# Kernel tuning notes

Measured on AMD Instinct MI355X. Metric: run time of the kernel, lower is better.

## Reference

```python
import jax, jax.numpy as jnp
import numpy as np

B, T, C = 2, 2048, 1024
N_HEAD = 16
HEAD_DIM = C // N_HEAD


def setup_inputs() -> dict:
    key = jax.random.key(0)
    k1, k2, k3 = jax.random.split(key, 3)
    s = 1.0 / np.sqrt(C)
    return {
        "x": jax.random.normal(k1, (B, T, C), dtype=jnp.float32),
        "w_qkv": jax.random.normal(k2, (C, 3 * C), dtype=jnp.float32) * s,
        "b_qkv": jnp.zeros((3 * C,), dtype=jnp.float32),
        "w_out": jax.random.normal(k3, (C, C), dtype=jnp.float32) * s,
        "b_out": jnp.zeros((C,), dtype=jnp.float32),
    }


def reference(x, w_qkv, b_qkv, w_out, b_out):
    b, t, c = x.shape
    qkv = x @ w_qkv + b_qkv                                   # [B,T,3C]
    # Faithful to torch: view(B,T,H,3*hd).transpose(1,2) then split last dim
    qkv = qkv.reshape(b, t, N_HEAD, 3 * HEAD_DIM).transpose(0, 2, 1, 3)  # [B,H,T,3hd]
    q, k, v = jnp.split(qkv, 3, axis=-1)                      # each [B,H,T,hd]
    att = jnp.einsum("bhqd,bhkd->bhqk", q, k) / np.sqrt(HEAD_DIM)
    causal = jnp.tril(jnp.ones((t, t), dtype=bool))
    att = jnp.where(causal[None, None], att, -jnp.inf)
    att = jax.nn.softmax(att, axis=-1)                        # dropout p=0 (eval)
    y = jnp.einsum("bhqk,bhkd->bhqd", att, v)                 # [B,H,T,hd]
    y = y.transpose(0, 2, 1, 3).reshape(b, t, c)
    return y @ w_out + b_out
```

## Files before the change

kernel.cpp:

```cpp
#include <hip/hip_runtime.h>


#define T_SEQ 2048
#define C_DIM 1024
#define NH    16
#define HD    64
#define BT    4096

typedef short bf16x8 __attribute__((ext_vector_type(8)));
typedef float floatx4 __attribute__((ext_vector_type(4)));

static __device__ __forceinline__ unsigned short f2bf(float f) {
    union { float f; unsigned u; } v; v.f = f;
    unsigned u = v.u;
    return (unsigned short)((u + 0x7FFFu + ((u >> 16) & 1u)) >> 16);
}
static __device__ __forceinline__ float bf2f(unsigned short u) {
    union { unsigned u; float f; } v; v.u = ((unsigned)u) << 16; return v.f;
}

static __device__ __forceinline__ void gl2lds16(const void* g, void* l) {
    __builtin_amdgcn_global_load_lds(
        (const __attribute__((address_space(1))) unsigned int*)g,
        (__attribute__((address_space(3))) unsigned int*)l, 16, 0, 0);
}

static __device__ __forceinline__ void transpose_body(float (*tile)[65],
                                                      const float* __restrict__ W,
                                                      unsigned short* __restrict__ Wt,
                                                      int K, int N, int bx, int by) {
    const int k0 = by << 6;
    const int n0 = bx << 6;
    const int rr = threadIdx.x >> 4;
    const int cc = (threadIdx.x & 15) << 2;
#pragma unroll
    for (int i = 0; i < 4; i++) {
        int r = rr + (i << 4);
        *(float4*)&tile[r][cc] = *(const float4*)(W + (size_t)(k0 + r) * N + n0 + cc);
    }
    __syncthreads();
#pragma unroll
    for (int i = 0; i < 4; i++) {
        int nr = rr + (i << 4);
        ushort4 o;
        o.x = f2bf(tile[cc + 0][nr]);
        o.y = f2bf(tile[cc + 1][nr]);
        o.z = f2bf(tile[cc + 2][nr]);
        o.w = f2bf(tile[cc + 3][nr]);
        *(ushort4*)(Wt + (size_t)(n0 + nr) * K + k0 + cc) = o;
    }
}

__global__ __launch_bounds__(256) void prep(const float* __restrict__ x,
                                            unsigned short* __restrict__ xb,
                                            const float* __restrict__ w_qkv,
                                            unsigned short* __restrict__ wqkvT,
                                            const float* __restrict__ w_out,
                                            unsigned short* __restrict__ woutT) {
    __shared__ float tile[64][65];
    const int bx = blockIdx.x;
    if (bx < 1024) {
        int i = (bx * 256 + threadIdx.x) * 4;
        const int n = BT * C_DIM;
        const int stride = 1024 * 1024;
        for (; i < n; i += stride) {
            float4 f = *(const float4*)(x + i);
            ushort4 o;
            o.x = f2bf(f.x); o.y = f2bf(f.y); o.z = f2bf(f.z); o.w = f2bf(f.w);
            *(ushort4*)(xb + i) = o;
        }
    } else if (bx < 1024 + 768) {
        int b = bx - 1024;
        transpose_body(tile, w_qkv, wqkvT, 1024, 3072, b % 48, b / 48);
    } else {
        int b = bx - 1024 - 768;
        transpose_body(tile, w_out, woutT, 1024, 1024, b % 16, b / 16);
    }
}

__global__ __launch_bounds__(256) void transp_v(const unsigned short* __restrict__ vb,
                                                unsigned short* __restrict__ vt) {
    __shared__ unsigned short tile[64][68];
    const int t0 = blockIdx.x << 6;
    const int bh = blockIdx.y;
    const size_t base = (size_t)bh * T_SEQ * HD;
    const int r = threadIdx.x >> 3;
    const int c = (threadIdx.x & 7) << 3;
#pragma unroll
    for (int i = 0; i < 2; i++) {
        const unsigned short* src = vb + base + (size_t)(t0 + r + (i << 5)) * HD + c;
        ushort4 u0 = *(const ushort4*)src;
        ushort4 u1 = *(const ushort4*)(src + 4);
        *(ushort4*)&tile[r + (i << 5)][c] = u0;
        *(ushort4*)&tile[r + (i << 5)][c + 4] = u1;
    }
    __syncthreads();
#pragma unroll
    for (int i = 0; i < 2; i++) {
        int s = threadIdx.x + (i << 8);
        int d = s >> 3;
        int tc = (s & 7) << 3;
        ushort4 o0, o1;
        o0.x = tile[tc + 0][d]; o0.y = tile[tc + 1][d];
        o0.z = tile[tc + 2][d]; o0.w = tile[tc + 3][d];
        o1.x = tile[tc + 4][d]; o1.y = tile[tc + 5][d];
        o1.z = tile[tc + 6][d]; o1.w = tile[tc + 7][d];
        unsigned short* dst = vt + ((size_t)bh * HD + d) * T_SEQ + t0 + tc;
        *(ushort4*)dst = o0;
        *(ushort4*)(dst + 4) = o1;
    }
}

#define GEMM_CORE(A_, Bt_, K_)                                                      \
    __shared__ short As[128 * 64];                                                  \
    __shared__ short Bs[128 * 64];                                                  \
    const int tid  = threadIdx.x;                                                   \
    const int lane = tid & 63, wave = tid >> 6;                                     \
    const int ln   = lane & 15, quad = lane >> 4;                                   \
    const int wm   = wave & 1,  wn   = wave >> 1;                                   \
    const int row0 = blockIdx.y << 7;                                               \
    const int col0 = blockIdx.x << 7;                                               \
    floatx4 acc[4][4];                                                              \
    _Pragma("unroll")                                                               \
    for (int i = 0; i < 4; i++)                                                     \
        _Pragma("unroll")                                                           \
        for (int j = 0; j < 4; j++) acc[i][j] = (floatx4){0.f, 0.f, 0.f, 0.f};      \
    for (int k0 = 0; k0 < K_; k0 += 64) {                                           \
        _Pragma("unroll")                                                           \
        for (int i = 0; i < 4; i++) {                                               \
            int c = (i << 8) + tid;                                                 \
            int r = c >> 3;                                                         \
            int gsrc = (c & 7) ^ (r & 7);                                           \
            gl2lds16(A_  + (size_t)(row0 + r) * K_ + k0 + (gsrc << 3), &As[c << 3]); \
            gl2lds16(Bt_ + (size_t)(col0 + r) * K_ + k0 + (gsrc << 3), &Bs[c << 3]); \
        }                                                                           \
        __syncthreads();                                                            \
        _Pragma("unroll")                                                           \
        for (int half = 0; half < 2; half++) {                                      \
            bf16x8 af[4], bfr[4];                                                   \
            _Pragma("unroll")                                                       \
            for (int t4 = 0; t4 < 4; t4++) {                                        \
                int ra = (wm << 6) + (t4 << 4) + ln;                                \
                int rb = (wn << 6) + (t4 << 4) + ln;                                \
                int g  = (half << 2) + quad;                                        \
                af[t4]  = *(bf16x8*)&As[((ra << 3) + (g ^ (ra & 7))) << 3];         \
                bfr[t4] = *(bf16x8*)&Bs[((rb << 3) + (g ^ (rb & 7))) << 3];         \
            }                                                                       \
            _Pragma("unroll")                                                       \
            for (int mt = 0; mt < 4; mt++)                                          \
                _Pragma("unroll")                                                   \
                for (int nt = 0; nt < 4; nt++)                                      \
                    acc[mt][nt] = __builtin_amdgcn_mfma_f32_16x16x32_bf16(af[mt], bfr[nt], acc[mt][nt], 0, 0, 0); \
        }                                                                           \
        __syncthreads();                                                            \
    }

__global__ __launch_bounds__(256) void gemm_qkv(const unsigned short* __restrict__ A,
                                                const unsigned short* __restrict__ Bt,
                                                const float* __restrict__ bias,
                                                unsigned short* __restrict__ qb,
                                                unsigned short* __restrict__ kb,
                                                unsigned short* __restrict__ vb) {
    GEMM_CORE(A, Bt, 1024)
#pragma unroll
    for (int mt = 0; mt < 4; mt++) {
#pragma unroll
        for (int nt = 0; nt < 4; nt++) {
            int n = col0 + (wn << 6) + (nt << 4) + ln;
            int h = n / 192, r = n % 192;
            int sel = r >> 6, d = r & 63;
            float bv = bias[n];
#pragma unroll
            for (int e = 0; e < 4; e++) {
                int m = row0 + (wm << 6) + (mt << 4) + (quad << 2) + e;
                int b = m >> 11, t = m & 2047;
                float val = acc[mt][nt][e] + bv;
                size_t idx = (((size_t)(b * NH + h)) * T_SEQ + t) * HD + d;
                if (sel == 0)
                    qb[idx] = f2bf(val * 0.125f);
                else if (sel == 1)
                    kb[idx] = f2bf(val);
                else
                    vb[idx] = f2bf(val);
            }
        }
    }
}

__global__ __launch_bounds__(256) void gemm_out(const unsigned short* __restrict__ A,
                                                const unsigned short* __restrict__ Bt,
                                                const float* __restrict__ bias,
                                                float* __restrict__ out) {
    const int K = 1024, N = 1024;
    __shared__ short As[128 * 64];
    __shared__ short Bs[64 * 64];
    const int tid  = threadIdx.x;
    const int lane = tid & 63, wave = tid >> 6;
    const int ln   = lane & 15, quad = lane >> 4;
    const int wm   = wave & 1,  wn   = wave >> 1;
    const int row0 = blockIdx.y << 7;
    const int col0 = blockIdx.x << 6;
    floatx4 acc[4][2];
#pragma unroll
    for (int i = 0; i < 4; i++)
#pragma unroll
        for (int j = 0; j < 2; j++) acc[i][j] = (floatx4){0.f, 0.f, 0.f, 0.f};
    for (int k0 = 0; k0 < K; k0 += 64) {
#pragma unroll
        for (int i = 0; i < 4; i++) {
            int c = (i << 8) + tid;
            int r = c >> 3;
            int gsrc = (c & 7) ^ (r & 7);
            gl2lds16(A + (size_t)(row0 + r) * K + k0 + (gsrc << 3), &As[c << 3]);
        }
#pragma unroll
        for (int i = 0; i < 2; i++) {
            int c = (i << 8) + tid;
            int r = c >> 3;
            int gsrc = (c & 7) ^ (r & 7);
            gl2lds16(Bt + (size_t)(col0 + r) * K + k0 + (gsrc << 3), &Bs[c << 3]);
        }
        __syncthreads();
#pragma unroll
        for (int half = 0; half < 2; half++) {
            bf16x8 af[4], bfr[2];
#pragma unroll
            for (int t4 = 0; t4 < 4; t4++) {
                int ra = (wm << 6) + (t4 << 4) + ln;
                int g  = (half << 2) + quad;
                af[t4] = *(bf16x8*)&As[((ra << 3) + (g ^ (ra & 7))) << 3];
            }
#pragma unroll
            for (int t2 = 0; t2 < 2; t2++) {
                int rb = (wn << 5) + (t2 << 4) + ln;
                int g  = (half << 2) + quad;
                bfr[t2] = *(bf16x8*)&Bs[((rb << 3) + (g ^ (rb & 7))) << 3];
            }
#pragma unroll
            for (int mt = 0; mt < 4; mt++)
#pragma unroll
                for (int nt = 0; nt < 2; nt++)
                    acc[mt][nt] = __builtin_amdgcn_mfma_f32_16x16x32_bf16(af[mt], bfr[nt], acc[mt][nt], 0, 0, 0);
        }
        __syncthreads();
    }
#pragma unroll
    for (int mt = 0; mt < 4; mt++) {
#pragma unroll
        for (int nt = 0; nt < 2; nt++) {
            int n = col0 + (wn << 5) + (nt << 4) + ln;
            float bv = bias[n];
#pragma unroll
            for (int e = 0; e < 4; e++) {
                int m = row0 + (wm << 6) + (mt << 4) + (quad << 2) + e;
                out[(size_t)m * N + n] = acc[mt][nt][e] + bv;
            }
        }
    }
}

__global__ __launch_bounds__(256, 4) void attn_p1(const unsigned short* __restrict__ qb,
                                                  const unsigned short* __restrict__ kb,
                                                  const unsigned short* __restrict__ vt,
                                                  unsigned short* __restrict__ y,
                                                  unsigned short* __restrict__ po,
                                                  float* __restrict__ pm,
                                                  float* __restrict__ pl) {
    __shared__ short Ks[64][72];
    __shared__ short Vs[64][72];
    __shared__ short QP[64][72];
    const int tid  = threadIdx.x;
    const int w    = tid >> 6, lane = tid & 63;
    const int ln   = lane & 15, quad = lane >> 4;
    const int bx   = blockIdx.x;
    int qt, cidx, kt_lo; bool fin;
    if (bx < 16)      { qt = 31 - bx;        cidx = 0; kt_lo = 0;  fin = false; }
    else if (bx < 32) { qt = 31 - (bx - 16); cidx = 1; kt_lo = 16; fin = false; }
    else              { qt = 15 - (bx - 32); cidx = 0; kt_lo = 0;  fin = true;  }
    const int kt_hi = (!fin && cidx == 0) ? 15 : qt;
    const int bh   = blockIdx.y;
    const size_t base = (size_t)bh * T_SEQ * HD;
    const int q0   = qt << 6;
    const int sb   = q0 + (w << 4);
    const float NEG_INF = -__builtin_inff();

    const int sr = tid >> 3;
    const int sc = (tid & 7) << 3;

    bf16x8 qtmp[2], kreg[2], vreg[2];
    const int kk0 = kt_lo << 6;
#pragma unroll
    for (int i = 0; i < 2; i++) {
        qtmp[i] = *(const bf16x8*)(qb + base + (size_t)(q0 + sr + (i << 5)) * HD + sc);
        kreg[i] = *(const bf16x8*)(kb + base + (size_t)(kk0 + sr + (i << 5)) * HD + sc);
        vreg[i] = *(const bf16x8*)(vt + base + (size_t)(sr + (i << 5)) * T_SEQ + kk0 + sc);
    }
#pragma unroll
    for (int i = 0; i < 2; i++) *(bf16x8*)&QP[sr + (i << 5)][sc] = qtmp[i];
    __syncthreads();

    bf16x8 bq0 = *(bf16x8*)&QP[(w << 4) + ln][quad << 3];
    bf16x8 bq1 = *(bf16x8*)&QP[(w << 4) + ln][32 + (quad << 3)];

    floatx4 o[4];
#pragma unroll
    for (int nt = 0; nt < 4; nt++) o[nt] = (floatx4){0.f, 0.f, 0.f, 0.f};
    float m_prev = NEG_INF, l_run = 0.f;

    for (int kt = kt_lo; kt <= kt_hi; kt++) {
        const int k0 = kt << 6;
        __syncthreads();
#pragma unroll
        for (int i = 0; i < 2; i++) {
            *(bf16x8*)&Ks[sr + (i << 5)][sc] = kreg[i];
            *(bf16x8*)&Vs[sr + (i << 5)][sc] = vreg[i];
        }
        __syncthreads();
        if (kt < kt_hi) {
            const int kn = k0 + 64;
#pragma unroll
            for (int i = 0; i < 2; i++) {
                kreg[i] = *(const bf16x8*)(kb + base + (size_t)(kn + sr + (i << 5)) * HD + sc);
                vreg[i] = *(const bf16x8*)(vt + base + (size_t)(sr + (i << 5)) * T_SEQ + kn + sc);
            }
        }

        const bool diag  = (kt == qt);
        const int  nlive = diag ? w : 3;

        floatx4 st[4];
#pragma unroll
        for (int ktl = 0; ktl < 4; ktl++) {
            if (ktl <= nlive) {
                bf16x8 a0 = *(bf16x8*)&Ks[(ktl << 4) + ln][quad << 3];
                bf16x8 a1 = *(bf16x8*)&Ks[(ktl << 4) + ln][32 + (quad << 3)];
                floatx4 acc = (floatx4){0.f, 0.f, 0.f, 0.f};
                acc = __builtin_amdgcn_mfma_f32_16x16x32_bf16(a0, bq0, acc, 0, 0, 0);
                acc = __builtin_amdgcn_mfma_f32_16x16x32_bf16(a1, bq1, acc, 0, 0, 0);
                st[ktl] = acc;
            }
        }
        if (diag) {
#pragma unroll
            for (int ktl = 0; ktl < 4; ktl++) {
                if (ktl <= nlive) {
#pragma unroll
                    for (int e = 0; e < 4; e++) {
                        int kg = k0 + (ktl << 4) + (quad << 2) + e;
                        if (kg > sb + ln) st[ktl][e] = NEG_INF;
                    }
                }
            }
        }

        float mx = NEG_INF;
#pragma unroll
        for (int ktl = 0; ktl < 4; ktl++)
            if (ktl <= nlive) {
#pragma unroll
                for (int e = 0; e < 4; e++) mx = fmaxf(mx, st[ktl][e]);
            }
        mx = fmaxf(mx, __shfl_xor(mx, 16));
        mx = fmaxf(mx, __shfl_xor(mx, 32));
        float m_new = fmaxf(m_prev, mx);
        float alpha = __expf(m_prev - m_new);
        float psum = 0.f;
#pragma unroll
        for (int ktl = 0; ktl < 4; ktl++)
            if (ktl <= nlive) {
#pragma unroll
                for (int e = 0; e < 4; e++) {
                    float p = __expf(st[ktl][e] - m_new);
                    st[ktl][e] = p;
                    psum += p;
                }
            }
        psum += __shfl_xor(psum, 16);
        psum += __shfl_xor(psum, 32);
        l_run = l_run * alpha + psum;
        m_prev = m_new;

#pragma unroll
        for (int ktl = 0; ktl < 4; ktl++) {
            ushort4 pw;
            if (ktl <= nlive) {
                pw.x = f2bf(st[ktl][0]); pw.y = f2bf(st[ktl][1]);
                pw.z = f2bf(st[ktl][2]); pw.w = f2bf(st[ktl][3]);
            } else {
                pw.x = 0; pw.y = 0; pw.z = 0; pw.w = 0;
            }
            *(ushort4*)&QP[(w << 4) + ln][(ktl << 4) + (quad << 2)] = pw;
        }

        float arow[4];
#pragma unroll
        for (int e = 0; e < 4; e++) arow[e] = __shfl(alpha, (quad << 2) + e);
#pragma unroll
        for (int nt = 0; nt < 4; nt++)
#pragma unroll
            for (int e = 0; e < 4; e++) o[nt][e] *= arow[e];

        bf16x8 ap0 = *(bf16x8*)&QP[(w << 4) + ln][quad << 3];
        bf16x8 ap1 = *(bf16x8*)&QP[(w << 4) + ln][32 + (quad << 3)];
#pragma unroll
        for (int nt = 0; nt < 4; nt++) {
            bf16x8 v0 = *(bf16x8*)&Vs[(nt << 4) + ln][quad << 3];
            bf16x8 v1 = *(bf16x8*)&Vs[(nt << 4) + ln][32 + (quad << 3)];
            o[nt] = __builtin_amdgcn_mfma_f32_16x16x32_bf16(ap0, v0, o[nt], 0, 0, 0);
            o[nt] = __builtin_amdgcn_mfma_f32_16x16x32_bf16(ap1, v1, o[nt], 0, 0, 0);
        }
    }

    if (fin) {
        float linv[4];
#pragma unroll
        for (int e = 0; e < 4; e++) linv[e] = 1.0f / __shfl(l_run, (quad << 2) + e);
        const int b = bh >> 4, h = bh & 15;
#pragma unroll
        for (int e = 0; e < 4; e++) {
            int t = sb + (quad << 2) + e;
            unsigned short* yrow = y + ((size_t)b * T_SEQ + t) * C_DIM + h * HD;
#pragma unroll
            for (int nt = 0; nt < 4; nt++)
                yrow[(nt << 4) + ln] = f2bf(o[nt][e] * linv[e]);
        }
    } else {
        const int slot = (((bh << 4) + (qt - 16)) << 1) + cidx;
        if (quad == 0) {
            pm[(slot << 6) + (w << 4) + ln] = m_prev;
            pl[(slot << 6) + (w << 4) + ln] = l_run;
        }
#pragma unroll
        for (int e = 0; e < 4; e++) {
            int q = (w << 4) + (quad << 2) + e;
            unsigned short* porow = po + (((size_t)slot << 6) + q) * HD;
#pragma unroll
            for (int nt = 0; nt < 4; nt++)
                porow[(nt << 4) + ln] = f2bf(o[nt][e]);
        }
    }
}

__global__ __launch_bounds__(256) void attn_p2(const unsigned short* __restrict__ po,
                                               const float* __restrict__ pm,
                                               const float* __restrict__ pl,
                                               unsigned short* __restrict__ y) {
    const int qt = 16 + blockIdx.x;
    const int bh = blockIdx.y;
    const int slot0 = ((bh << 4) + (qt - 16)) << 1;
    const int tid = threadIdx.x;
    const int q  = tid >> 2;
    const int d0 = (tid & 3) << 4;
    float m0 = pm[(slot0 << 6) + q], m1 = pm[((slot0 + 1) << 6) + q];
    float l0 = pl[(slot0 << 6) + q], l1 = pl[((slot0 + 1) << 6) + q];
    float m  = fmaxf(m0, m1);
    float a0 = __expf(m0 - m), a1 = __expf(m1 - m);
    float inv = 1.0f / (l0 * a0 + l1 * a1);
    a0 *= inv; a1 *= inv;
    const unsigned short* r0 = po + (((size_t)slot0 << 6) + q) * HD + d0;
    const unsigned short* r1 = po + (((size_t)(slot0 + 1) << 6) + q) * HD + d0;
    const int b = bh >> 4, h = bh & 15;
    const int t = (qt << 6) + q;
    unsigned short* yrow = y + ((size_t)b * T_SEQ + t) * C_DIM + h * HD + d0;
#pragma unroll
    for (int i = 0; i < 4; i++) {
        ushort4 u0 = *(const ushort4*)(r0 + (i << 2));
        ushort4 u1 = *(const ushort4*)(r1 + (i << 2));
        ushort4 ow;
        ow.x = f2bf(bf2f(u0.x) * a0 + bf2f(u1.x) * a1);
        ow.y = f2bf(bf2f(u0.y) * a0 + bf2f(u1.y) * a1);
        ow.z = f2bf(bf2f(u0.z) * a0 + bf2f(u1.z) * a1);
        ow.w = f2bf(bf2f(u0.w) * a0 + bf2f(u1.w) * a1);
        *(ushort4*)(yrow + (i << 2)) = ow;
    }
}

extern "C" void kernel_launch(void* const* d_in, const int* in_sizes, int n_in,
                              void* d_out, int out_size, void* d_ws, size_t ws_size,
                              hipStream_t stream) {
    (void)in_sizes; (void)n_in; (void)out_size; (void)ws_size;
    const float* x     = (const float*)d_in[0];
    const float* w_qkv = (const float*)d_in[1];
    const float* b_qkv = (const float*)d_in[2];
    const float* w_out = (const float*)d_in[3];
    const float* b_out = (const float*)d_in[4];
    float* out = (float*)d_out;

    char* ws = (char*)d_ws;
    unsigned short* qb    = (unsigned short*)ws;
    unsigned short* kb    = (unsigned short*)(ws + ((size_t)8  << 20));
    unsigned short* vb    = (unsigned short*)(ws + ((size_t)16 << 20));
    unsigned short* vt    = (unsigned short*)(ws + ((size_t)24 << 20));
    unsigned short* xb    = (unsigned short*)(ws + ((size_t)32 << 20));
    unsigned short* yb    = xb;
    unsigned short* wqkvT = (unsigned short*)(ws + ((size_t)40 << 20));
    unsigned short* woutT = (unsigned short*)(ws + ((size_t)46 << 20));
    unsigned short* po    = (unsigned short*)(ws + ((size_t)48 << 20));
    float*          pm    = (float*)(ws + ((size_t)56 << 20));
    float*          pl    = (float*)(ws + ((size_t)56 << 20) + (256 << 10));

    prep    <<<2048, 256, 0, stream>>>(x, xb, w_qkv, wqkvT, w_out, woutT);
    gemm_qkv<<<dim3(24, 32), 256, 0, stream>>>(xb, wqkvT, b_qkv, qb, kb, vb);
    transp_v<<<dim3(32, 32), 256, 0, stream>>>(vb, vt);
    attn_p1 <<<dim3(48, 32), 256, 0, stream>>>(qb, kb, vt, yb, po, pm, pl);
    attn_p2 <<<dim3(16, 32), 256, 0, stream>>>(po, pm, pl, yb);
    gemm_out<<<dim3(16, 32), 256, 0, stream>>>(yb, woutT, b_out, out);
}
```

Baseline: 210.1 us.

## Fuse V transpose into QKV GEMM epilogue and double-buffer K/V in attention

The separate V-transpose kernel is removed. The QKV GEMM epilogue now stages V values in shared memory and writes them directly in transposed [bh][d][t] layout, saving a launch and a full read/write of V. The attention kernel double-buffers K/V tiles in LDS, cutting one barrier per iteration. It also loads Q fragments straight from global into registers and lowers the occupancy hint from 4 to 3 blocks, which grows LDS use and may reduce occupancy.

```diff
diff --git a/kernel.cpp b/kernel.cpp
--- a/kernel.cpp
+++ b/kernel.cpp
@@ -75,39 +75,6 @@
     } else {
         int b = bx - 1024 - 768;
         transpose_body(tile, w_out, woutT, 1024, 1024, b % 16, b / 16);
-    }
-}
-
-__global__ __launch_bounds__(256) void transp_v(const unsigned short* __restrict__ vb,
-                                                unsigned short* __restrict__ vt) {
-    __shared__ unsigned short tile[64][68];
-    const int t0 = blockIdx.x << 6;
-    const int bh = blockIdx.y;
-    const size_t base = (size_t)bh * T_SEQ * HD;
-    const int r = threadIdx.x >> 3;
-    const int c = (threadIdx.x & 7) << 3;
-#pragma unroll
-    for (int i = 0; i < 2; i++) {
-        const unsigned short* src = vb + base + (size_t)(t0 + r + (i << 5)) * HD + c;
-        ushort4 u0 = *(const ushort4*)src;
-        ushort4 u1 = *(const ushort4*)(src + 4);
-        *(ushort4*)&tile[r + (i << 5)][c] = u0;
-        *(ushort4*)&tile[r + (i << 5)][c + 4] = u1;
-    }
-    __syncthreads();
-#pragma unroll
-    for (int i = 0; i < 2; i++) {
-        int s = threadIdx.x + (i << 8);
-        int d = s >> 3;
-        int tc = (s & 7) << 3;
-        ushort4 o0, o1;
-        o0.x = tile[tc + 0][d]; o0.y = tile[tc + 1][d];
-        o0.z = tile[tc + 2][d]; o0.w = tile[tc + 3][d];
-        o1.x = tile[tc + 4][d]; o1.y = tile[tc + 5][d];
-        o1.z = tile[tc + 6][d]; o1.w = tile[tc + 7][d];
-        unsigned short* dst = vt + ((size_t)bh * HD + d) * T_SEQ + t0 + tc;
-        *(ushort4*)dst = o0;
-        *(ushort4*)(dst + 4) = o1;
     }
 }
 
@@ -160,29 +127,45 @@
                                                 const float* __restrict__ bias,
                                                 unsigned short* __restrict__ qb,
                                                 unsigned short* __restrict__ kb,
-                                                unsigned short* __restrict__ vb) {
+                                                unsigned short* __restrict__ vt) {
     GEMM_CORE(A, Bt, 1024)
+    const int bmod = blockIdx.x % 3;
 #pragma unroll
     for (int mt = 0; mt < 4; mt++) {
 #pragma unroll
         for (int nt = 0; nt < 4; nt++) {
-            int n = col0 + (wn << 6) + (nt << 4) + ln;
+            int lc = (wn << 6) + (nt << 4) + ln;
+            int n = col0 + lc;
             int h = n / 192, r = n % 192;
             int sel = r >> 6, d = r & 63;
             float bv = bias[n];
 #pragma unroll
             for (int e = 0; e < 4; e++) {
-                int m = row0 + (wm << 6) + (mt << 4) + (quad << 2) + e;
+                int m_loc = (wm << 6) + (mt << 4) + (quad << 2) + e;
+                int m = row0 + m_loc;
                 int b = m >> 11, t = m & 2047;
                 float val = acc[mt][nt][e] + bv;
-                size_t idx = (((size_t)(b * NH + h)) * T_SEQ + t) * HD + d;
-                if (sel == 0)
-                    qb[idx] = f2bf(val * 0.125f);
-                else if (sel == 1)
-                    kb[idx] = f2bf(val);
-                else
-                    vb[idx] = f2bf(val);
-            }
+                if (sel == 0) {
+                    qb[(((size_t)(b * NH + h)) * T_SEQ + t) * HD + d] = f2bf(val * 0.125f);
+                } else if (sel == 1) {
+                    kb[(((size_t)(b * NH + h)) * T_SEQ + t) * HD + d] = f2bf(val);
+                } else {
+                    As[(d << 7) + m_loc] = (short)f2bf(val);
+                }
+            }
+        }
+    }
+    if (bmod != 0) {
+        __syncthreads();
+        const int h  = (col0 + ((bmod == 1) ? 0 : 64)) / 192;
+        const int b  = row0 >> 11, t0 = row0 & 2047;
+        unsigned short* vbase = vt + ((size_t)(b * NH + h) * HD) * T_SEQ + t0;
+#pragma unroll
+        for (int i = 0; i < 4; i++) {
+            int c = (i << 8) + tid;
+            int d = c >> 4, ch = c & 15;
+            bf16x8 vv = *(bf16x8*)&As[(d << 7) + (ch << 3)];
+            *(bf16x8*)(vbase + (size_t)d * T_SEQ + (ch << 3)) = vv;
         }
     }
 }
@@ -259,16 +242,16 @@
     }
 }
 
-__global__ __launch_bounds__(256, 4) void attn_p1(const unsigned short* __restrict__ qb,
+__global__ __launch_bounds__(256, 3) void attn_p1(const unsigned short* __restrict__ qb,
                                                   const unsigned short* __restrict__ kb,
                                                   const unsigned short* __restrict__ vt,
                                                   unsigned short* __restrict__ y,
                                                   unsigned short* __restrict__ po,
                                                   float* __restrict__ pm,
                                                   float* __restrict__ pl) {
-    __shared__ short Ks[64][72];
-    __shared__ short Vs[64][72];
-    __shared__ short QP[64][72];
+    __shared__ short Ks[2][64][72];
+    __shared__ short Vs[2][64][72];
+    __shared__ short P[64][72];
     const int tid  = threadIdx.x;
     const int w    = tid >> 6, lane = tid & 63;
     const int ln   = lane & 15, quad = lane >> 4;
@@ -287,20 +270,33 @@
     const int sr = tid >> 3;
     const int sc = (tid & 7) << 3;
 
-    bf16x8 qtmp[2], kreg[2], vreg[2];
-    const int kk0 = kt_lo << 6;
-#pragma unroll
-    for (int i = 0; i < 2; i++) {
-        qtmp[i] = *(const bf16x8*)(qb + base + (size_t)(q0 + sr + (i << 5)) * HD + sc);
-        kreg[i] = *(const bf16x8*)(kb + base + (size_t)(kk0 + sr + (i << 5)) * HD + sc);
-        vreg[i] = *(const bf16x8*)(vt + base + (size_t)(sr + (i << 5)) * T_SEQ + kk0 + sc);
-    }
-#pragma unroll
-    for (int i = 0; i < 2; i++) *(bf16x8*)&QP[sr + (i << 5)][sc] = qtmp[i];
+    const unsigned short* qrow = qb + base + (size_t)(sb + ln) * HD;
+    const bf16x8 bq0 = *(const bf16x8*)(qrow + (quad << 3));
+    const bf16x8 bq1 = *(const bf16x8*)(qrow + 32 + (quad << 3));
+
+    bf16x8 kreg[2], vreg[2];
+    {
+        const int kk = kt_lo << 6;
+#pragma unroll
+        for (int i = 0; i < 2; i++) {
+            kreg[i] = *(const bf16x8*)(kb + base + (size_t)(kk + sr + (i << 5)) * HD + sc);
+            vreg[i] = *(const bf16x8*)(vt + base + (size_t)(sr + (i << 5)) * T_SEQ + kk + sc);
+        }
+#pragma unroll
+        for (int i = 0; i < 2; i++) {
+            *(bf16x8*)&Ks[0][sr + (i << 5)][sc] = kreg[i];
+            *(bf16x8*)&Vs[0][sr + (i << 5)][sc] = vreg[i];
+        }
+        if (kt_lo < kt_hi) {
+            const int kk2 = (kt_lo + 1) << 6;
+#pragma unroll
+            for (int i = 0; i < 2; i++) {
+                kreg[i] = *(const bf16x8*)(kb + base + (size_t)(kk2 + sr + (i << 5)) * HD + sc);
+                vreg[i] = *(const bf16x8*)(vt + base + (size_t)(sr + (i << 5)) * T_SEQ + kk2 + sc);
+            }
+        }
+    }
     __syncthreads();
-
-    bf16x8 bq0 = *(bf16x8*)&QP[(w << 4) + ln][quad << 3];
-    bf16x8 bq1 = *(bf16x8*)&QP[(w << 4) + ln][32 + (quad << 3)];
 
     floatx4 o[4];
 #pragma unroll
@@ -308,20 +304,22 @@
     float m_prev = NEG_INF, l_run = 0.f;
 
     for (int kt = kt_lo; kt <= kt_hi; kt++) {
+        const int cur = (kt - kt_lo) & 1;
         const int k0 = kt << 6;
-        __syncthreads();
-#pragma unroll
-        for (int i = 0; i < 2; i++) {
-            *(bf16x8*)&Ks[sr + (i << 5)][sc] = kreg[i];
-            *(bf16x8*)&Vs[sr + (i << 5)][sc] = vreg[i];
-        }
-        __syncthreads();
         if (kt < kt_hi) {
-            const int kn = k0 + 64;
+            const int nxt = cur ^ 1;
 #pragma unroll
             for (int i = 0; i < 2; i++) {
-                kreg[i] = *(const bf16x8*)(kb + base + (size_t)(kn + sr + (i << 5)) * HD + sc);
-                vreg[i] = *(const bf16x8*)(vt + base + (size_t)(sr + (i << 5)) * T_SEQ + kn + sc);
+                *(bf16x8*)&Ks[nxt][sr + (i << 5)][sc] = kreg[i];
+                *(bf16x8*)&Vs[nxt][sr + (i << 5)][sc] = vreg[i];
+            }
+            if (kt + 1 < kt_hi) {
+                const int kk2 = (kt + 2) << 6;
+#pragma unroll
+                for (int i = 0; i < 2; i++) {
+                    kreg[i] = *(const bf16x8*)(kb + base + (size_t)(kk2 + sr + (i << 5)) * HD + sc);
+                    vreg[i] = *(const bf16x8*)(vt + base + (size_t)(sr + (i << 5)) * T_SEQ + kk2 + sc);
+                }
             }
         }
 
@@ -332,8 +330,8 @@
 #pragma unroll
         for (int ktl = 0; ktl < 4; ktl++) {
             if (ktl <= nlive) {
-                bf16x8 a0 = *(bf16x8*)&Ks[(ktl << 4) + ln][quad << 3];
-                bf16x8 a1 = *(bf16x8*)&Ks[(ktl << 4) + ln][32 + (quad << 3)];
+                bf16x8 a0 = *(bf16x8*)&Ks[cur][(ktl << 4) + ln][quad << 3];
+                bf16x8 a1 = *(bf16x8*)&Ks[cur][(ktl << 4) + ln][32 + (quad << 3)];
                 floatx4 acc = (floatx4){0.f, 0.f, 0.f, 0.f};
                 acc = __builtin_amdgcn_mfma_f32_16x16x32_bf16(a0, bq0, acc, 0, 0, 0);
                 acc = __builtin_amdgcn_mfma_f32_16x16x32_bf16(a1, bq1, acc, 0, 0, 0);
@@ -389,7 +387,7 @@
             } else {
                 pw.x = 0; pw.y = 0; pw.z = 0; pw.w = 0;
             }
-            *(ushort4*)&QP[(w << 4) + ln][(ktl << 4) + (quad << 2)] = pw;
+            *(ushort4*)&P[(w << 4) + ln][(ktl << 4) + (quad << 2)] = pw;
         }
 
         float arow[4];
@@ -400,15 +398,16 @@
 #pragma unroll
             for (int e = 0; e < 4; e++) o[nt][e] *= arow[e];
 
-        bf16x8 ap0 = *(bf16x8*)&QP[(w << 4) + ln][quad << 3];
-        bf16x8 ap1 = *(bf16x8*)&QP[(w << 4) + ln][32 + (quad << 3)];
+        bf16x8 ap0 = *(bf16x8*)&P[(w << 4) + ln][quad << 3];
+        bf16x8 ap1 = *(bf16x8*)&P[(w << 4) + ln][32 + (quad << 3)];
 #pragma unroll
         for (int nt = 0; nt < 4; nt++) {
-            bf16x8 v0 = *(bf16x8*)&Vs[(nt << 4) + ln][quad << 3];
-            bf16x8 v1 = *(bf16x8*)&Vs[(nt << 4) + ln][32 + (quad << 3)];
+            bf16x8 v0 = *(bf16x8*)&Vs[cur][(nt << 4) + ln][quad << 3];
+            bf16x8 v1 = *(bf16x8*)&Vs[cur][(nt << 4) + ln][32 + (quad << 3)];
             o[nt] = __builtin_amdgcn_mfma_f32_16x16x32_bf16(ap0, v0, o[nt], 0, 0, 0);
             o[nt] = __builtin_amdgcn_mfma_f32_16x16x32_bf16(ap1, v1, o[nt], 0, 0, 0);
         }
+        __syncthreads();
     }
 
     if (fin) {
@@ -489,19 +488,17 @@
     char* ws = (char*)d_ws;
     unsigned short* qb    = (unsigned short*)ws;
     unsigned short* kb    = (unsigned short*)(ws + ((size_t)8  << 20));
-    unsigned short* vb    = (unsigned short*)(ws + ((size_t)16 << 20));
-    unsigned short* vt    = (unsigned short*)(ws + ((size_t)24 << 20));
-    unsigned short* xb    = (unsigned short*)(ws + ((size_t)32 << 20));
+    unsigned short* vt    = (unsigned short*)(ws + ((size_t)16 << 20));
+    unsigned short* xb    = (unsigned short*)(ws + ((size_t)24 << 20));
     unsigned short* yb    = xb;
-    unsigned short* wqkvT = (unsigned short*)(ws + ((size_t)40 << 20));
-    unsigned short* woutT = (unsigned short*)(ws + ((size_t)46 << 20));
-    unsigned short* po    = (unsigned short*)(ws + ((size_t)48 << 20));
-    float*          pm    = (float*)(ws + ((size_t)56 << 20));
-    float*          pl    = (float*)(ws + ((size_t)56 << 20) + (256 << 10));
+    unsigned short* wqkvT = (unsigned short*)(ws + ((size_t)32 << 20));
+    unsigned short* woutT = (unsigned short*)(ws + ((size_t)38 << 20));
+    unsigned short* po    = (unsigned short*)(ws + ((size_t)40 << 20));
+    float*          pm    = (float*)(ws + ((size_t)48 << 20));
+    float*          pl    = (float*)(ws + ((size_t)48 << 20) + (256 << 10));
 
     prep    <<<2048, 256, 0, stream>>>(x, xb, w_qkv, wqkvT, w_out, woutT);
-    gemm_qkv<<<dim3(24, 32), 256, 0, stream>>>(xb, wqkvT, b_qkv, qb, kb, vb);
-    transp_v<<<dim3(32, 32), 256, 0, stream>>>(vb, vt);
+    gemm_qkv<<<dim3(24, 32), 256, 0, stream>>>(xb, wqkvT, b_qkv, qb, kb, vt);
     attn_p1 <<<dim3(48, 32), 256, 0, stream>>>(qb, kb, vt, yb, po, pm, pl);
     attn_p2 <<<dim3(16, 32), 256, 0, stream>>>(po, pm, pl, yb);
     gemm_out<<<dim3(16, 32), 256, 0, stream>>>(yb, woutT, b_out, out);
```

Measured after the change: 220.1 us. +4.8%, slower.
